# Performance work log

Measured on AMD Instinct MI355X. Metric: run time of the kernel, lower is better.

The kernel has to match this reference:

```python
import jax, jax.numpy as jnp
import numpy as np

K = 16          # patch_size
P2 = 256        # patch_size**2
D_PD = 512      # learned base dictionary atoms (D_out_lam_pd)
D_LAM = 112     # adaptive atoms from sdict, = 8*14 (D_out_lam)
DD = D_PD + D_LAM  # 624
T = 5
INDICE = 112
MIN_V, MAX_V = 0.0, 1.0


def _idx(H, W, k, stride):
    oh = (H - k) // stride + 1
    ow = (W - k) // stride + 1
    r = jnp.arange(k)[:, None] + stride * jnp.arange(oh)[None, :]  # [k, oh]
    c = jnp.arange(k)[:, None] + stride * jnp.arange(ow)[None, :]  # [k, ow]
    return r[:, None, :, None], c[None, :, None, :], oh, ow


def _unfold(x, k, stride):
    # torch.nn.Unfold: [N, C*k*k, L] with (C, kh, kw) channel order, row-major L
    N, C, H, W = x.shape
    r, c, oh, ow = _idx(H, W, k, stride)
    return x[:, :, r, c].reshape(N, C * k * k, oh * ow)


def _fold(p, H, W, k):
    # torch.nn.functional.fold (col2im) with stride 1, overlap-add
    N, ckk, L = p.shape
    r, c, oh, ow = _idx(H, W, k, 1)
    C = ckk // (k * k)
    out = jnp.zeros((N, C, H, W), p.dtype)
    return out.at[:, :, r, c].add(p.reshape(N, C, k, k, oh, ow))


def _mlp(x, ws):
    # Linear + clamp(min=0) chain, no relu after last layer (dropout = eval identity)
    for w, b in ws[:-1]:
        x = jnp.maximum(x @ w + b, 0.0)
    w, b = ws[-1]
    return x @ w + b


def _cbam(x, w1, w2, conv_w):
    # standard CBAM: channel attention (shared MLP on avg+max pool) then 7x7 spatial attention
    def mlp(v):
        return jnp.maximum(v @ w1, 0.0) @ w2
    ca = jax.nn.sigmoid(mlp(x.mean(axis=(2, 3))) + mlp(x.max(axis=(2, 3))))
    x = x * ca[:, :, None, None]
    s = jnp.stack([x.mean(axis=1), x.max(axis=1)], axis=1)  # [N,2,h,w]
    sa = jax.lax.conv_general_dilated(s, conv_w, (1, 1), [(3, 3), (3, 3)],
                                      dimension_numbers=('NCHW', 'OIHW', 'NCHW'))
    return x * jax.nn.sigmoid(sa)


def _soft(x, l):
    return jnp.sign(x) * jnp.maximum(jnp.abs(x) - l, 0.0)


def _stage(img, Dict, c, sd_ws, ca1, ca2, saw, lam_ws, pd_ws, w_ws):
    N, C, H, W = img.shape
    uf = _unfold(img, K, 1).transpose(0, 2, 1)     # [N, L, 256]
    uf1 = _unfold(img, K, 8).transpose(0, 2, 1)    # [N, L1, 256]
    step = uf1.shape[1] // INDICE                  # static under jit
    ext = uf1[:, ::step, :][:, :INDICE, :]         # [N, 112, 256]
    sd = _mlp(ext, sd_ws)                          # linears1..4
    sd = sd / jnp.maximum(jnp.linalg.norm(sd, axis=-1, keepdims=True), 1e-12)
    sd = _cbam(sd.transpose(0, 2, 1).reshape(N, P2, 8, 14), ca1, ca2, saw)
    sd = sd.reshape(N, P2, INDICE)                 # [N, 256, 112]
    Dcat = jnp.concatenate([jnp.broadcast_to(Dict, (N,) + Dict.shape), sd], axis=-1)  # [N,256,624]
    # thresholds: l = cat(lpd, ls)
    thr = jnp.concatenate([_mlp(uf, pd_ws) / c, _mlp(uf, lam_ws) / c], axis=-1)  # [N,L,624]
    y = uf @ Dcat                                  # [N, L, 624]
    # S = (I - D^T D / c)^T; D^T D is symmetric so the transpose is a no-op
    S = jnp.eye(DD, dtype=img.dtype) - (Dcat.transpose(0, 2, 1) @ Dcat) / c
    z = _soft(y, thr)
    for _ in range(T):  # LISTA unrolled iterations (T static)
        z = _soft(z @ S + y / c, thr)
    Wg = jax.nn.sigmoid(_mlp(uf, w_ws))            # [N, L, 256]
    x_pred = jnp.clip(z @ Dcat.transpose(0, 2, 1), MIN_V, MAX_V) * Wg
    num = _fold(x_pred.transpose(0, 2, 1), H, W, K)
    den = _fold(Wg.transpose(0, 2, 1), H, W, K)    # fold of W * ones
    return num / den


def _forward(x, Dict, c, s1w, s1b, s2w, s2b, s3w, s3b, s4w, s4b, caw1, caw2, saw,
             a1w, a1b, a2w, a2b, a3w, a3b, p1w, p1b, p2w, p2b, p3w, p3b,
             b1w, b1b, b2w, b2b, b3w, b3b, q1w, q1b, q2w, q2b, q3w, q3b,
             w1w, w1b, w2w, w2b, w3w, w3b):
    sd_ws = [(s1w, s1b), (s2w, s2b), (s3w, s3b), (s4w, s4b)]
    w_ws = [(w1w, w1b), (w2w, w2b), (w3w, w3b)]
    res = _stage(x, Dict, c, sd_ws, caw1, caw2, saw,
                 [(a1w, a1b), (a2w, a2b), (a3w, a3b)],
                 [(p1w, p1b), (p2w, p2b), (p3w, p3b)], w_ws)
    res = _stage(res, Dict, c, sd_ws, caw1, caw2, saw,
                 [(b1w, b1b), (b2w, b2b), (b3w, b3b)],
                 [(q1w, q1b), (q2w, q2b), (q3w, q3b)], w_ws)
    return res


def setup_inputs() -> dict:
    key = jax.random.key(0)
    ks = iter(jax.random.split(key, 40))
    d = {}
    d['x'] = jax.random.uniform(next(ks), (2, 1, 128, 128), jnp.float32)
    Dm = jax.random.normal(next(ks), (P2, D_PD), jnp.float32)
    d['Dict'] = Dm / jnp.linalg.norm(Dm, axis=0, keepdims=True)  # unit-norm atoms
    d['c'] = jnp.asarray(10.0, jnp.float32)  # c > ||D^T D||_2
    dims = {'s1': (256, 512), 's2': (512, 1024), 's3': (1024, 512), 's4': (512, 256),
            'a1': (256, 1024), 'a2': (1024, 512), 'a3': (512, 112),
            'p1': (256, 1024), 'p2': (1024, 512), 'p3': (512, 512),
            'b1': (256, 1024), 'b2': (1024, 512), 'b3': (512, 112),
            'q1': (256, 1024), 'q2': (1024, 512), 'q3': (512, 512),
            'w1': (256, 1024), 'w2': (1024, 512), 'w3': (512, 256)}
    for name, (i, o) in dims.items():
        d[name + 'w'] = jax.random.normal(next(ks), (i, o), jnp.float32) / np.float32(np.sqrt(i))
        d[name + 'b'] = jnp.zeros((o,), jnp.float32)
    d['caw1'] = jax.random.normal(next(ks), (256, 512), jnp.float32) / np.float32(16.0)
    d['caw2'] = jax.random.normal(next(ks), (512, 256), jnp.float32) / np.float32(np.sqrt(512))
    d['saw'] = jax.random.normal(next(ks), (1, 2, 7, 7), jnp.float32) * np.float32(0.1)
    return d


def reference(x, Dict, c, s1w, s1b, s2w, s2b, s3w, s3b, s4w, s4b, caw1, caw2, saw,
              a1w, a1b, a2w, a2b, a3w, a3b, p1w, p1b, p2w, p2b, p3w, p3b,
              b1w, b1b, b2w, b2b, b3w, b3b, q1w, q1b, q2w, q2b, q3w, q3b,
              w1w, w1b, w2w, w2b, w3w, w3b):
    return _forward(x, Dict, c, s1w, s1b, s2w, s2b, s3w, s3b, s4w, s4b, caw1, caw2, saw,
                    a1w, a1b, a2w, a2b, a3w, a3b, p1w, p1b, p2w, p2b, p3w, p3b,
                    b1w, b1b, b2w, b2b, b3w, b3b, q1w, q1b, q2w, q2b, q3w, q3b,
                    w1w, w1b, w2w, w2b, w3w, w3b)
```

## Files before the change

### kernel.cpp

```cpp
#include <hip/hip_runtime.h>
#include <hip/hip_bf16.h>
#include <math.h>

#define L_LOC 12769
#define NB 2
#define NLR (NB * L_LOC)

typedef short short8v __attribute__((ext_vector_type(8)));
typedef float f32x4 __attribute__((ext_vector_type(4)));
typedef __hip_bfloat16 bf16;

__device__ __forceinline__ float softf(float x, float l) {
  float a = fmaxf(fabsf(x) - l, 0.0f);
  return x > 0.0f ? a : (x < 0.0f ? -a : 0.0f);
}
__device__ __forceinline__ float sigf(float x) { return 1.0f / (1.0f + expf(-x)); }
__device__ __forceinline__ void split2(float v, bf16& h, bf16& l) {
  h = __float2bfloat16(v);
  l = __float2bfloat16(v - __bfloat162float(h));
}

__global__ __launch_bounds__(256) void sdmlp_k(
    const float* __restrict__ img,
    const float* __restrict__ w1, const float* __restrict__ b1,
    const float* __restrict__ w2, const float* __restrict__ b2,
    const float* __restrict__ w3, const float* __restrict__ b3,
    const float* __restrict__ w4, const float* __restrict__ b4,
    float* __restrict__ sd)
{
  __shared__ float A_[4][1024];
  __shared__ float B_[4][1024];
  __shared__ float red[4][4];
  const int r0 = blockIdx.x * 4;
  const int t = threadIdx.x;
#pragma unroll
  for (int rr = 0; rr < 4; ++rr) {
    int r = r0 + rr;
    int n = r / 112, e = r - n * 112;
    int l1 = 2 * e, i1 = l1 / 15, j1 = l1 - i1 * 15;
    A_[rr][t] = img[n * 16384 + (8 * i1 + (t >> 4)) * 128 + 8 * j1 + (t & 15)];
  }
  __syncthreads();
  {
    float acc[4][2];
#pragma unroll
    for (int rr = 0; rr < 4; ++rr) { acc[rr][0] = b1[t]; acc[rr][1] = b1[t + 256]; }
#pragma unroll 4
    for (int k = 0; k < 256; ++k) {
      float w0 = w1[k * 512 + t], w1v = w1[k * 512 + t + 256];
#pragma unroll
      for (int rr = 0; rr < 4; ++rr) {
        float a = A_[rr][k];
        acc[rr][0] = fmaf(a, w0, acc[rr][0]);
        acc[rr][1] = fmaf(a, w1v, acc[rr][1]);
      }
    }
#pragma unroll
    for (int rr = 0; rr < 4; ++rr) {
      B_[rr][t] = fmaxf(acc[rr][0], 0.0f);
      B_[rr][t + 256] = fmaxf(acc[rr][1], 0.0f);
    }
  }
  __syncthreads();
  {
    float acc[4][4];
#pragma unroll
    for (int rr = 0; rr < 4; ++rr)
#pragma unroll
      for (int j = 0; j < 4; ++j) acc[rr][j] = b2[t + j * 256];
#pragma unroll 4
    for (int k = 0; k < 512; ++k) {
      float w0 = w2[k * 1024 + t], w1v = w2[k * 1024 + t + 256];
      float w2v = w2[k * 1024 + t + 512], w3v = w2[k * 1024 + t + 768];
#pragma unroll
      for (int rr = 0; rr < 4; ++rr) {
        float a = B_[rr][k];
        acc[rr][0] = fmaf(a, w0, acc[rr][0]);
        acc[rr][1] = fmaf(a, w1v, acc[rr][1]);
        acc[rr][2] = fmaf(a, w2v, acc[rr][2]);
        acc[rr][3] = fmaf(a, w3v, acc[rr][3]);
      }
    }
    __syncthreads();
#pragma unroll
    for (int rr = 0; rr < 4; ++rr)
#pragma unroll
      for (int j = 0; j < 4; ++j) A_[rr][t + j * 256] = fmaxf(acc[rr][j], 0.0f);
  }
  __syncthreads();
  {
    float acc[4][2];
#pragma unroll
    for (int rr = 0; rr < 4; ++rr) { acc[rr][0] = b3[t]; acc[rr][1] = b3[t + 256]; }
#pragma unroll 4
    for (int k = 0; k < 1024; ++k) {
      float w0 = w3[k * 512 + t], w1v = w3[k * 512 + t + 256];
#pragma unroll
      for (int rr = 0; rr < 4; ++rr) {
        float a = A_[rr][k];
        acc[rr][0] = fmaf(a, w0, acc[rr][0]);
        acc[rr][1] = fmaf(a, w1v, acc[rr][1]);
      }
    }
    __syncthreads();
#pragma unroll
    for (int rr = 0; rr < 4; ++rr) {
      B_[rr][t] = fmaxf(acc[rr][0], 0.0f);
      B_[rr][t + 256] = fmaxf(acc[rr][1], 0.0f);
    }
  }
  __syncthreads();
  float v[4];
#pragma unroll
  for (int rr = 0; rr < 4; ++rr) v[rr] = b4[t];
#pragma unroll 4
  for (int k = 0; k < 512; ++k) {
    float w = w4[k * 256 + t];
#pragma unroll
    for (int rr = 0; rr < 4; ++rr) v[rr] = fmaf(B_[rr][k], w, v[rr]);
  }
  float ss[4];
#pragma unroll
  for (int rr = 0; rr < 4; ++rr) ss[rr] = v[rr] * v[rr];
#pragma unroll
  for (int o = 1; o < 64; o <<= 1)
#pragma unroll
    for (int rr = 0; rr < 4; ++rr) ss[rr] += __shfl_xor(ss[rr], o);
  if ((t & 63) == 0)
#pragma unroll
    for (int rr = 0; rr < 4; ++rr) red[t >> 6][rr] = ss[rr];
  __syncthreads();
#pragma unroll
  for (int rr = 0; rr < 4; ++rr) {
    float s = red[0][rr] + red[1][rr] + red[2][rr] + red[3][rr];
    float sc = 1.0f / fmaxf(sqrtf(s), 1e-12f);
    sd[(r0 + rr) * 256 + t] = v[rr] * sc;
  }
}

enum { ME_RELU = 0, ME_SCALE = 1, ME_SIG = 2, ME_Y = 3, ME_SOFT = 4, ME_XP = 5, ME_SMAT = 6 };

template <int EPI, int TERMS, int WLO>
__global__ __launch_bounds__(256) void mgemm_k(
    const bf16* __restrict__ A, int lda, size_t aOff,
    const bf16* __restrict__ B0, const bf16* __restrict__ B1, int ldb, size_t bOff,
    void* __restrict__ Cv, int ldc, size_t cOff,
    bf16* __restrict__ Zp,
    const float* __restrict__ bias,
    const float* __restrict__ E1, const float* __restrict__ E2, int lde,
    const float* __restrict__ cptr, int bRow, int Rc, int r0, int N, int K)
{
  const int NPA = (TERMS >= 3) ? 2 : 1;
  const int NPB = (TERMS >= 2) ? 2 : 1;
  __shared__ char As[(TERMS >= 3) ? 2 : 1][8192];
  __shared__ char Bs[(TERMS >= 2) ? 2 : 1][8192];
  const int t = threadIdx.x;
  const int lane = t & 63, wv = t >> 6;
  const int wr = wv >> 1, wc = wv & 1;
  const int m0 = blockIdx.x * 128, n0 = blockIdx.y * 128;
  const int nb = (m0 >= bRow) ? 1 : 0;
  const bf16* __restrict__ Bt = nb ? B1 : B0;
  const int row16 = lane & 15, kg = lane >> 4;
  const int grow = t >> 2;
  const int gcol = (t & 3) * 8;
  f32x4 acc[4][4];
#pragma unroll
  for (int i = 0; i < 4; ++i)
#pragma unroll
    for (int j = 0; j < 4; ++j) { acc[i][j][0] = 0.f; acc[i][j][1] = 0.f; acc[i][j][2] = 0.f; acc[i][j][3] = 0.f; }

  for (int k0 = 0; k0 < K; k0 += 32) {
#pragma unroll
    for (int h = 0; h < NPA; ++h)
#pragma unroll
      for (int i = 0; i < 2; ++i) {
        const bf16* ga = A + h * aOff + (size_t)(m0 + i * 64 + grow) * lda + k0 + gcol;
        __builtin_amdgcn_global_load_lds(
            (const __attribute__((address_space(1))) void*)ga,
            (__attribute__((address_space(3))) void*)(As[h] + i * 4096 + wv * 1024), 16, 0, 0);
      }
#pragma unroll
    for (int h = 0; h < NPB; ++h)
#pragma unroll
      for (int i = 0; i < 2; ++i) {
        const bf16* gb = Bt + h * bOff + (size_t)(n0 + i * 64 + grow) * ldb + k0 + gcol;
        __builtin_amdgcn_global_load_lds(
            (const __attribute__((address_space(1))) void*)gb,
            (__attribute__((address_space(3))) void*)(Bs[h] + i * 4096 + wv * 1024), 16, 0, 0);
      }
    __syncthreads();
    short8v ah[4], al[4], bh[4], bl[4];
#pragma unroll
    for (int mi = 0; mi < 4; ++mi) {
      int o = (wr * 64 + mi * 16 + row16) * 64 + kg * 16;
      ah[mi] = *(const short8v*)(As[0] + o);
      if (TERMS >= 3) al[mi] = *(const short8v*)(As[NPA - 1] + o);
    }
#pragma unroll
    for (int ni = 0; ni < 4; ++ni) {
      int o = (wc * 64 + ni * 16 + row16) * 64 + kg * 16;
      bh[ni] = *(const short8v*)(Bs[0] + o);
      if (TERMS >= 2) bl[ni] = *(const short8v*)(Bs[NPB - 1] + o);
    }
#pragma unroll
    for (int mi = 0; mi < 4; ++mi)
#pragma unroll
      for (int ni = 0; ni < 4; ++ni) {
        if (TERMS >= 2)
          acc[mi][ni] = __builtin_amdgcn_mfma_f32_16x16x32_bf16(ah[mi], bl[ni], acc[mi][ni], 0, 0, 0);
        if (TERMS >= 3)
          acc[mi][ni] = __builtin_amdgcn_mfma_f32_16x16x32_bf16(al[mi], bh[ni], acc[mi][ni], 0, 0, 0);
        acc[mi][ni] = __builtin_amdgcn_mfma_f32_16x16x32_bf16(ah[mi], bh[ni], acc[mi][ni], 0, 0, 0);
      }
    __syncthreads();
  }

  float invc = 1.0f;
  if (EPI == ME_SCALE || EPI == ME_SOFT || EPI == ME_SMAT) invc = 1.0f / cptr[0];
  bf16* Cb = (bf16*)Cv;
  float* Cf = (float*)Cv;
#pragma unroll
  for (int ni = 0; ni < 4; ++ni) {
    int col = n0 + wc * 64 + ni * 16 + row16;
    const bool colok = col < N;
    float bv = 0.0f;
    if ((EPI == ME_RELU || EPI == ME_SCALE || EPI == ME_SIG) && colok) bv = bias[col];
#pragma unroll
    for (int mi = 0; mi < 4; ++mi) {
      int rowb = m0 + wr * 64 + mi * 16 + kg * 4;
#pragma unroll
      for (int r = 0; r < 4; ++r) {
        int row = rowb + r;
        float v = acc[mi][ni][r];
        if (EPI == ME_RELU) {
          if (colok) {
            float o = fmaxf(v + bv, 0.0f);
            size_t ci = (size_t)row * ldc + col;
            if (WLO) {
              bf16 h, l; split2(o, h, l);
              Cb[ci] = h; Cb[ci + cOff] = l;
            } else {
              Cb[ci] = __float2bfloat16(o);
            }
          }
        } else if (EPI == ME_SCALE) {
          if (colok) Cf[(size_t)row * ldc + col] = (v + bv) * invc;
        } else if (EPI == ME_SIG) {
          if (colok) {
            int rl = row - nb * bRow;
            if (rl < Rc && rl >= 0)
              Cf[(size_t)col * NLR + (size_t)nb * L_LOC + r0 + rl] = sigf(v + bv);
          }
        } else if (EPI == ME_Y) {
          if (colok) {
            size_t e = (size_t)row * lde + col;
            Cf[(size_t)row * ldc + col] = v;
            Zp[(size_t)row * 640 + col] = __float2bfloat16(softf(v, E1[e]));
          }
        } else if (EPI == ME_SOFT) {
          if (colok) {
            size_t e = (size_t)row * lde + col;
            Cb[(size_t)row * ldc + col] = __float2bfloat16(softf(v + E1[e] * invc, E2[e]));
          }
        } else if (EPI == ME_XP) {
          int rl = row - nb * bRow;
          if (colok && rl < Rc && rl >= 0) {
            size_t g = (size_t)col * NLR + (size_t)nb * L_LOC + r0 + rl;
            Cf[g] = fminf(fmaxf(v, 0.0f), 1.0f) * E1[g];
          }
        } else {
          if (row < Rc && colok)
            Cf[(size_t)row * ldc + col] = (row == col ? 1.0f : 0.0f) - v * invc;
        }
      }
    }
  }
}

static void mgemm(hipStream_t st, int EPI, int wlo,
                  const bf16* A, int lda, size_t aOff,
                  const bf16* B0, const bf16* B1, int ldb, size_t bOff,
                  void* C, int ldc, size_t cOff,
                  bf16* Zp,
                  const float* bias, const float* E1, const float* E2, int lde,
                  const float* cptr, int bRow, int Rc, int r0,
                  int Mp, int N, int K)
{
  dim3 grid(Mp / 128, (N + 127) / 128), blk(256);
#define MG(ep, tm, wl) mgemm_k<ep, tm, wl><<<grid, blk, 0, st>>>(A, lda, aOff, B0, B1, ldb, bOff, C, ldc, cOff, Zp, bias, E1, E2, lde, cptr, bRow, Rc, r0, N, K)
  switch (EPI) {
    case ME_RELU:  if (wlo) MG(ME_RELU, 1, 1); else MG(ME_RELU, 1, 0); break;
    case ME_SCALE: MG(ME_SCALE, 3, 0); break;
    case ME_SIG:   MG(ME_SIG, 1, 0); break;
    case ME_Y:     MG(ME_Y, 3, 0); break;
    case ME_SOFT:  MG(ME_SOFT, 2, 0); break;
    case ME_XP:    MG(ME_XP, 2, 0); break;
    case ME_SMAT:  MG(ME_SMAT, 3, 0); break;
  }
#undef MG
}

struct WTable {
  const float* src[15];
  bf16* dst[15];
  int K[15], N[15], Kp[15], Np[15];
  int base[16];
};

__global__ void wtransall_k(WTable w) {
  int idx = blockIdx.x * 256 + threadIdx.x;
  if (idx >= w.base[15]) return;
  int s = 0;
  while (s < 14 && idx >= w.base[s + 1]) ++s;
  int li = idx - w.base[s];
  int Kp = w.Kp[s];
  int n = li / Kp, k = li - n * Kp;
  float v = (n < w.N[s] && k < w.K[s]) ? w.src[s][(size_t)k * w.N[s] + n] : 0.0f;
  bf16 h, l; split2(v, h, l);
  w.dst[s][li] = h;
  w.dst[s][li + (size_t)w.Np[s] * Kp] = l;
}

__global__ void dcatconv_k(const float* __restrict__ Dict, const float* __restrict__ Dc,
                           bf16* __restrict__ Db, bf16* __restrict__ DbT) {
  int idx = blockIdx.x * 256 + threadIdx.x;
  if (idx >= 327680) return;
  int n = idx / 163840, r = idx - n * 163840;
  int p = r / 640, a = r - p * 640;
  float v = 0.0f;
  if (a < 512)      v = Dict[p * 512 + a];
  else if (a < 624) v = Dc[(size_t)n * 159744 + p * 624 + a];
  bf16 h, l; split2(v, h, l);
  size_t base = (size_t)n * 327680;
  Db[base + p * 640 + a] = h;
  Db[base + 163840 + p * 640 + a] = l;
  DbT[base + (size_t)a * 256 + p] = h;
  DbT[base + 163840 + (size_t)a * 256 + p] = l;
}

__global__ void sconv_k(const float* __restrict__ Sf, bf16* __restrict__ Sb) {
  int idx = blockIdx.x * 256 + threadIdx.x;
  if (idx >= 819200) return;
  int n = idx / 409600, r = idx - n * 409600;
  int i = r / 640, j = r - i * 640;
  float v = (i < 624 && j < 624) ? Sf[(size_t)n * 389376 + i * 624 + j] : 0.0f;
  bf16 h, l; split2(v, h, l);
  size_t base = (size_t)n * 819200;
  Sb[base + r] = h; Sb[base + 409600 + r] = l;
}

__global__ void unfold_k(const float* __restrict__ img, bf16* __restrict__ uf,
                         int r0, int Rc, int bRowc, size_t pOff) {
  int bi = blockIdx.x;
  int nb = bi >= Rc;
  int rl = nb ? bi - Rc : bi;
  int row = nb * bRowc + rl;
  int p = threadIdx.x;
  int l = r0 + rl;
  int i0 = l / 113, j0 = l - i0 * 113;
  float v = img[nb * 16384 + (i0 + (p >> 4)) * 128 + j0 + (p & 15)];
  bf16 h, lo; split2(v, h, lo);
  size_t o = (size_t)row * 256 + p;
  uf[o] = h; uf[o + pOff] = lo;
}

__global__ __launch_bounds__(1024) void cbam_k(
    const float* __restrict__ sd, const float* __restrict__ w1,
    const float* __restrict__ w2, const float* __restrict__ saw,
    float* __restrict__ Dcat)
{
  __shared__ float mv[512], xv[512], hm[1024], hx[1024], ca[512];
  __shared__ float smean[224], smax[224];
  const int t = threadIdx.x;
  if (t < 512) {
    int n = t >> 8, ch = t & 255;
    float s = 0.0f, m = -INFINITY;
    for (int e = 0; e < 112; ++e) {
      float v = sd[(n * 112 + e) * 256 + ch];
      s += v; m = fmaxf(m, v);
    }
    mv[t] = s * (1.0f / 112.0f);
    xv[t] = m;
  }
  __syncthreads();
  {
    int n = t >> 9, o = t & 511;
    float sm = 0.0f, sx = 0.0f;
    for (int i = 0; i < 256; ++i) {
      float w = w1[i * 512 + o];
      sm += mv[n * 256 + i] * w;
      sx += xv[n * 256 + i] * w;
    }
    hm[t] = fmaxf(sm, 0.0f);
    hx[t] = fmaxf(sx, 0.0f);
  }
  __syncthreads();
  if (t < 512) {
    int n = t >> 8, ch = t & 255;
    float s = 0.0f;
    for (int o = 0; o < 512; ++o) s += (hm[n * 512 + o] + hx[n * 512 + o]) * w2[o * 256 + ch];
    ca[t] = sigf(s);
  }
  __syncthreads();
  if (t < 224) {
    int n = t / 112, s = t % 112;
    float sum = 0.0f, mx = -INFINITY;
    for (int ch = 0; ch < 256; ++ch) {
      float v = sd[(n * 112 + s) * 256 + ch] * ca[n * 256 + ch];
      Dcat[(size_t)n * 159744 + ch * 624 + 512 + s] = v;
      sum += v; mx = fmaxf(mx, v);
    }
    smean[t] = sum * (1.0f / 256.0f);
    smax[t] = mx;
  }
  __syncthreads();
  if (t < 224) {
    int n = t / 112, s = t % 112;
    int h = s / 14, w = s % 14;
    float acc = 0.0f;
    for (int dh = 0; dh < 7; ++dh) {
      int hh = h + dh - 3; if (hh < 0 || hh >= 8) continue;
      for (int dw = 0; dw < 7; ++dw) {
        int ww = w + dw - 3; if (ww < 0 || ww >= 14) continue;
        int sp = hh * 14 + ww;
        acc += smean[n * 112 + sp] * saw[dh * 7 + dw] + smax[n * 112 + sp] * saw[49 + dh * 7 + dw];
      }
    }
    float sg = sigf(acc);
    for (int ch = 0; ch < 256; ++ch) Dcat[(size_t)n * 159744 + ch * 624 + 512 + s] *= sg;
  }
}

__global__ void folddiv_k(const float* __restrict__ xpT, const float* __restrict__ wgT,
                          float* __restrict__ out) {
  int idx = blockIdx.x * 256 + threadIdx.x;
  if (idx >= 32768) return;
  int n = idx >> 14, rem = idx & 16383;
  int i = rem >> 7, j = rem & 127;
  float num = 0.0f, den = 0.0f;
  int kh0 = (i - 112 > 0) ? i - 112 : 0;
  int kh1 = (i < 15) ? i : 15;
  int kw0 = (j - 112 > 0) ? j - 112 : 0;
  int kw1 = (j < 15) ? j : 15;
  for (int kh = kh0; kh <= kh1; ++kh)
    for (int kw = kw0; kw <= kw1; ++kw) {
      int l = (i - kh) * 113 + (j - kw);
      size_t base = (size_t)(kh * 16 + kw) * NLR + (size_t)n * L_LOC + l;
      num += xpT[base];
      den += wgT[base];
    }
  out[idx] = num / den;
}

struct Bufs {
  float *xp, *wg, *Dcat_f, *S_f, *sd, *res;
  bf16 *Db, *DbT, *Sb;
  bf16 *uf, *h1, *h2, *z, *zn;
  float *thr, *y;
  size_t ufO, h1O, h2O;
  int R;
};

static void run_stage(hipStream_t st, const float* const* in, const float* img,
                      float* outimg, int pd0, int lam0,
                      bf16* const* WtPd, bf16* const* WtLam, bf16* const* WtW,
                      const Bufs& b)
{
  const float* cptr = in[2];
  sdmlp_k<<<dim3(56), dim3(256), 0, st>>>(img, in[3], in[4], in[5], in[6],
                                          in[7], in[8], in[9], in[10], b.sd);
  cbam_k<<<dim3(1), dim3(1024), 0, st>>>(b.sd, in[41], in[42], in[43], b.Dcat_f);
  dcatconv_k<<<dim3(1280), dim3(256), 0, st>>>(in[1], b.Dcat_f, b.Db, b.DbT);
  for (int n = 0; n < NB; ++n) {
    const bf16* Dt = b.DbT + (size_t)n * 327680;
    mgemm(st, ME_SMAT, 0, Dt, 256, 163840, Dt, Dt, 256, 163840,
          b.S_f + (size_t)n * 389376, 624, 0, 0,
          0, 0, 0, 0, cptr, 1 << 30, 624, 0, 640, 624, 256);
  }
  sconv_k<<<dim3(3200), dim3(256), 0, st>>>(b.S_f, b.Sb);

  for (int r0 = 0; r0 < L_LOC; r0 += b.R) {
    int Rc = L_LOC - r0; if (Rc > b.R) Rc = b.R;
    int bRowc = ((Rc + 127) / 128) * 128;
    int Mp = 2 * bRowc;
    unfold_k<<<dim3(2 * Rc), dim3(256), 0, st>>>(img, b.uf, r0, Rc, bRowc, b.ufO);
    mgemm(st, ME_RELU, 0, b.uf, 256, b.ufO, WtPd[0], WtPd[0], 256, 1024 * 256, b.h1, 1024, b.h1O,
          0, in[pd0 + 1], 0, 0, 0, cptr, bRowc, Rc, r0, Mp, 1024, 256);
    mgemm(st, ME_RELU, 1, b.h1, 1024, b.h1O, WtPd[1], WtPd[1], 1024, 512 * 1024, b.h2, 512, b.h2O,
          0, in[pd0 + 3], 0, 0, 0, cptr, bRowc, Rc, r0, Mp, 512, 1024);
    mgemm(st, ME_SCALE, 0, b.h2, 512, b.h2O, WtPd[2], WtPd[2], 512, 512 * 512, b.thr, 640, 0,
          0, in[pd0 + 5], 0, 0, 0, cptr, bRowc, Rc, r0, Mp, 512, 512);
    mgemm(st, ME_RELU, 0, b.uf, 256, b.ufO, WtLam[0], WtLam[0], 256, 1024 * 256, b.h1, 1024, b.h1O,
          0, in[lam0 + 1], 0, 0, 0, cptr, bRowc, Rc, r0, Mp, 1024, 256);
    mgemm(st, ME_RELU, 1, b.h1, 1024, b.h1O, WtLam[1], WtLam[1], 1024, 512 * 1024, b.h2, 512, b.h2O,
          0, in[lam0 + 3], 0, 0, 0, cptr, bRowc, Rc, r0, Mp, 512, 1024);
    mgemm(st, ME_SCALE, 0, b.h2, 512, b.h2O, WtLam[2], WtLam[2], 512, 128 * 512, b.thr + 512, 640, 0,
          0, in[lam0 + 5], 0, 0, 0, cptr, bRowc, Rc, r0, Mp, 112, 512);
    mgemm(st, ME_RELU, 0, b.uf, 256, b.ufO, WtW[0], WtW[0], 256, 1024 * 256, b.h1, 1024, b.h1O,
          0, in[36], 0, 0, 0, cptr, bRowc, Rc, r0, Mp, 1024, 256);
    mgemm(st, ME_RELU, 1, b.h1, 1024, b.h1O, WtW[1], WtW[1], 1024, 512 * 1024, b.h2, 512, b.h2O,
          0, in[38], 0, 0, 0, cptr, bRowc, Rc, r0, Mp, 512, 1024);
    mgemm(st, ME_SIG, 0, b.h2, 512, b.h2O, WtW[2], WtW[2], 512, 256 * 512, b.wg, 0, 0,
          0, in[40], 0, 0, 0, cptr, bRowc, Rc, r0, Mp, 256, 512);
    mgemm(st, ME_Y, 0, b.uf, 256, b.ufO, b.DbT, b.DbT + 327680, 256, 163840, b.y, 640, 0,
          b.z, 0, b.thr, 0, 640, cptr, bRowc, Rc, r0, Mp, 624, 256);
    bf16* zi = b.z; bf16* zo = b.zn;
    for (int it = 0; it < 5; ++it) {
      mgemm(st, ME_SOFT, 0, zi, 640, 0, b.Sb, b.Sb + 819200, 640, 409600, zo, 640, 0,
            0, 0, b.y, b.thr, 640, cptr, bRowc, Rc, r0, Mp, 624, 640);
      bf16* tmp = zi; zi = zo; zo = tmp;
    }
    mgemm(st, ME_XP, 0, zi, 640, 0, b.Db, b.Db + 327680, 640, 163840, b.xp, 0, 0,
          0, 0, b.wg, 0, 0, cptr, bRowc, Rc, r0, Mp, 256, 640);
  }
  folddiv_k<<<dim3(128), dim3(256), 0, st>>>(b.xp, b.wg, outimg);
}

extern "C" void kernel_launch(void* const* d_in, const int* in_sizes, int n_in,
                              void* d_out, int out_size, void* d_ws, size_t ws_size,
                              hipStream_t stream)
{
  (void)in_sizes; (void)n_in; (void)out_size;
  const float* const* in = (const float* const*)d_in;
  char* base = (char*)d_ws;
  size_t off = 0;
  auto allocf = [&](size_t nelem) -> float* {
    float* p = (float*)(base + off);
    off += ((nelem * 4 + 255) / 256) * 256;
    return p;
  };
  auto allocb2 = [&](size_t nelem) -> bf16* {
    bf16* p = (bf16*)(base + off);
    off += ((nelem * 2 * 2 + 255) / 256) * 256;
    return p;
  };
  auto allocb1 = [&](size_t nelem) -> bf16* {
    bf16* p = (bf16*)(base + off);
    off += ((nelem * 2 + 255) / 256) * 256;
    return p;
  };
  Bufs b;
  b.xp = allocf((size_t)NLR * 256);
  b.wg = allocf((size_t)NLR * 256);
  b.Dcat_f = allocf(2 * 256 * 624);
  b.S_f = allocf(2 * 624 * 624);
  b.sd = allocf(224 * 256);
  b.res = allocf(2 * 16384);
  b.Db = allocb2(2 * 163840);
  b.DbT = allocb2(2 * 163840);
  b.Sb = allocb2(2 * 409600);

  bf16 *Wa[3], *Wp[3], *Wb[3], *Wq[3], *Ww[3];
  struct WDesc { bf16** slot; int inIdx; int K, N, Kp, Np; };
  WDesc wd[15] = {
    {&Wa[0], 11, 256, 1024, 256, 1024}, {&Wa[1], 13, 1024, 512, 1024, 512}, {&Wa[2], 15, 512, 112, 512, 128},
    {&Wp[0], 17, 256, 1024, 256, 1024}, {&Wp[1], 19, 1024, 512, 1024, 512}, {&Wp[2], 21, 512, 512, 512, 512},
    {&Wb[0], 23, 256, 1024, 256, 1024}, {&Wb[1], 25, 1024, 512, 1024, 512}, {&Wb[2], 27, 512, 112, 512, 128},
    {&Wq[0], 29, 256, 1024, 256, 1024}, {&Wq[1], 31, 1024, 512, 1024, 512}, {&Wq[2], 33, 512, 512, 512, 512},
    {&Ww[0], 35, 256, 1024, 256, 1024}, {&Ww[1], 37, 1024, 512, 1024, 512}, {&Ww[2], 39, 512, 256, 512, 256},
  };
  WTable wt;
  int tot = 0;
  for (int i = 0; i < 15; ++i) {
    *wd[i].slot = allocb2((size_t)wd[i].Np * wd[i].Kp);
    wt.src[i] = in[wd[i].inIdx];
    wt.dst[i] = *wd[i].slot;
    wt.K[i] = wd[i].K; wt.N[i] = wd[i].N; wt.Kp[i] = wd[i].Kp; wt.Np[i] = wd[i].Np;
    wt.base[i] = tot;
    tot += wd[i].Np * wd[i].Kp;
  }
  wt.base[15] = tot;
  wtransall_k<<<dim3((tot + 255) / 256), dim3(256), 0, stream>>>(wt);

  long long avail = (long long)ws_size - (long long)off - (1 << 20);
  long long perrow2 = 2LL * (12800 + 64);
  int R = 12800;
  if (avail / perrow2 < 12800) R = (int)(avail / perrow2);
  R &= ~127;
  if (R < 128) R = 128;
  b.R = R;
  size_t rows2 = (size_t)2 * R;
  b.uf = allocb2(rows2 * 256);  b.ufO = rows2 * 256;
  b.h1 = allocb1(rows2 * 1024); b.h1O = 0;
  b.h2 = allocb2(rows2 * 512);  b.h2O = rows2 * 512;
  b.z = allocb1(rows2 * 640);
  b.zn = allocb1(rows2 * 640);
  b.thr = allocf(rows2 * 640);
  b.y = allocf(rows2 * 640);

  run_stage(stream, in, in[0], b.res, 17, 11, Wp, Wa, Ww, b);
  run_stage(stream, in, b.res, (float*)d_out, 29, 23, Wq, Wb, Ww, b);
}
```

Baseline: 3.260 ms.

## Fuse first-layer MLP GEMMs, move sdict MLP to MFMA, fold S conversion into epilogue

```diff
diff --git a/kernel.cpp b/kernel.cpp
--- a/kernel.cpp
+++ b/kernel.cpp
@@ -5,6 +5,7 @@
 #define L_LOC 12769
 #define NB 2
 #define NLR (NB * L_LOC)
+#define NW 20
 
 typedef short short8v __attribute__((ext_vector_type(8)));
 typedef float f32x4 __attribute__((ext_vector_type(4)));
@@ -20,125 +21,8 @@
   l = __float2bfloat16(v - __bfloat162float(h));
 }
 
-__global__ __launch_bounds__(256) void sdmlp_k(
-    const float* __restrict__ img,
-    const float* __restrict__ w1, const float* __restrict__ b1,
-    const float* __restrict__ w2, const float* __restrict__ b2,
-    const float* __restrict__ w3, const float* __restrict__ b3,
-    const float* __restrict__ w4, const float* __restrict__ b4,
-    float* __restrict__ sd)
-{
-  __shared__ float A_[4][1024];
-  __shared__ float B_[4][1024];
-  __shared__ float red[4][4];
-  const int r0 = blockIdx.x * 4;
-  const int t = threadIdx.x;
-#pragma unroll
-  for (int rr = 0; rr < 4; ++rr) {
-    int r = r0 + rr;
-    int n = r / 112, e = r - n * 112;
-    int l1 = 2 * e, i1 = l1 / 15, j1 = l1 - i1 * 15;
-    A_[rr][t] = img[n * 16384 + (8 * i1 + (t >> 4)) * 128 + 8 * j1 + (t & 15)];
-  }
-  __syncthreads();
-  {
-    float acc[4][2];
-#pragma unroll
-    for (int rr = 0; rr < 4; ++rr) { acc[rr][0] = b1[t]; acc[rr][1] = b1[t + 256]; }
-#pragma unroll 4
-    for (int k = 0; k < 256; ++k) {
-      float w0 = w1[k * 512 + t], w1v = w1[k * 512 + t + 256];
-#pragma unroll
-      for (int rr = 0; rr < 4; ++rr) {
-        float a = A_[rr][k];
-        acc[rr][0] = fmaf(a, w0, acc[rr][0]);
-        acc[rr][1] = fmaf(a, w1v, acc[rr][1]);
-      }
-    }
-#pragma unroll
-    for (int rr = 0; rr < 4; ++rr) {
-      B_[rr][t] = fmaxf(acc[rr][0], 0.0f);
-      B_[rr][t + 256] = fmaxf(acc[rr][1], 0.0f);
-    }
-  }
-  __syncthreads();
-  {
-    float acc[4][4];
-#pragma unroll
-    for (int rr = 0; rr < 4; ++rr)
-#pragma unroll
-      for (int j = 0; j < 4; ++j) acc[rr][j] = b2[t + j * 256];
-#pragma unroll 4
-    for (int k = 0; k < 512; ++k) {
-      float w0 = w2[k * 1024 + t], w1v = w2[k * 1024 + t + 256];
-      float w2v = w2[k * 1024 + t + 512], w3v = w2[k * 1024 + t + 768];
-#pragma unroll
-      for (int rr = 0; rr < 4; ++rr) {
-        float a = B_[rr][k];
-        acc[rr][0] = fmaf(a, w0, acc[rr][0]);
-        acc[rr][1] = fmaf(a, w1v, acc[rr][1]);
-        acc[rr][2] = fmaf(a, w2v, acc[rr][2]);
-        acc[rr][3] = fmaf(a, w3v, acc[rr][3]);
-      }
-    }
-    __syncthreads();
-#pragma unroll
-    for (int rr = 0; rr < 4; ++rr)
-#pragma unroll
-      for (int j = 0; j < 4; ++j) A_[rr][t + j * 256] = fmaxf(acc[rr][j], 0.0f);
-  }
-  __syncthreads();
-  {
-    float acc[4][2];
-#pragma unroll
-    for (int rr = 0; rr < 4; ++rr) { acc[rr][0] = b3[t]; acc[rr][1] = b3[t + 256]; }
-#pragma unroll 4
-    for (int k = 0; k < 1024; ++k) {
-      float w0 = w3[k * 512 + t], w1v = w3[k * 512 + t + 256];
-#pragma unroll
-      for (int rr = 0; rr < 4; ++rr) {
-        float a = A_[rr][k];
-        acc[rr][0] = fmaf(a, w0, acc[rr][0]);
-        acc[rr][1] = fmaf(a, w1v, acc[rr][1]);
-      }
-    }
-    __syncthreads();
-#pragma unroll
-    for (int rr = 0; rr < 4; ++rr) {
-      B_[rr][t] = fmaxf(acc[rr][0], 0.0f);
-      B_[rr][t + 256] = fmaxf(acc[rr][1], 0.0f);
-    }
-  }
-  __syncthreads();
-  float v[4];
-#pragma unroll
-  for (int rr = 0; rr < 4; ++rr) v[rr] = b4[t];
-#pragma unroll 4
-  for (int k = 0; k < 512; ++k) {
-    float w = w4[k * 256 + t];
-#pragma unroll
-    for (int rr = 0; rr < 4; ++rr) v[rr] = fmaf(B_[rr][k], w, v[rr]);
-  }
-  float ss[4];
-#pragma unroll
-  for (int rr = 0; rr < 4; ++rr) ss[rr] = v[rr] * v[rr];
-#pragma unroll
-  for (int o = 1; o < 64; o <<= 1)
-#pragma unroll
-    for (int rr = 0; rr < 4; ++rr) ss[rr] += __shfl_xor(ss[rr], o);
-  if ((t & 63) == 0)
-#pragma unroll
-    for (int rr = 0; rr < 4; ++rr) red[t >> 6][rr] = ss[rr];
-  __syncthreads();
-#pragma unroll
-  for (int rr = 0; rr < 4; ++rr) {
-    float s = red[0][rr] + red[1][rr] + red[2][rr] + red[3][rr];
-    float sc = 1.0f / fmaxf(sqrtf(s), 1e-12f);
-    sd[(r0 + rr) * 256 + t] = v[rr] * sc;
-  }
-}
-
-enum { ME_RELU = 0, ME_SCALE = 1, ME_SIG = 2, ME_Y = 3, ME_SOFT = 4, ME_XP = 5, ME_SMAT = 6 };
+enum { ME_RELU = 0, ME_SCALE = 1, ME_SIG = 2, ME_Y = 3, ME_SOFT = 4, ME_XP = 5,
+       ME_SMAT = 6, ME_LIN = 7 };
 
 template <int EPI, int TERMS, int WLO>
 __global__ __launch_bounds__(256) void mgemm_k(
@@ -224,7 +108,8 @@
     int col = n0 + wc * 64 + ni * 16 + row16;
     const bool colok = col < N;
     float bv = 0.0f;
-    if ((EPI == ME_RELU || EPI == ME_SCALE || EPI == ME_SIG) && colok) bv = bias[col];
+    if ((EPI == ME_RELU || EPI == ME_SCALE || EPI == ME_SIG || EPI == ME_LIN) && colok)
+      bv = bias[col];
 #pragma unroll
     for (int mi = 0; mi < 4; ++mi) {
       int rowb = m0 + wr * 64 + mi * 16 + kg * 4;
@@ -243,6 +128,8 @@
               Cb[ci] = __float2bfloat16(o);
             }
           }
+        } else if (EPI == ME_LIN) {
+          if (colok && row < Rc) Cf[(size_t)row * ldc + col] = v + bv;
         } else if (EPI == ME_SCALE) {
           if (colok) Cf[(size_t)row * ldc + col] = (v + bv) * invc;
         } else if (EPI == ME_SIG) {
@@ -269,15 +156,17 @@
             Cf[g] = fminf(fmaxf(v, 0.0f), 1.0f) * E1[g];
           }
         } else {
-          if (row < Rc && colok)
-            Cf[(size_t)row * ldc + col] = (row == col ? 1.0f : 0.0f) - v * invc;
+          float o = (row < 624 && col < 624) ? ((row == col ? 1.0f : 0.0f) - v * invc) : 0.0f;
+          bf16 h, l; split2(o, h, l);
+          size_t ci = (size_t)row * ldc + col;
+          Cb[ci] = h; Cb[ci + cOff] = l;
         }
       }
     }
   }
 }
 
-static void mgemm(hipStream_t st, int EPI, int wlo,
+static void mgemm(hipStream_t st, int EPI, int terms, int wlo,
                   const bf16* A, int lda, size_t aOff,
                   const bf16* B0, const bf16* B1, int ldb, size_t bOff,
                   void* C, int ldc, size_t cOff,
@@ -288,37 +177,74 @@
 {
   dim3 grid(Mp / 128, (N + 127) / 128), blk(256);
 #define MG(ep, tm, wl) mgemm_k<ep, tm, wl><<<grid, blk, 0, st>>>(A, lda, aOff, B0, B1, ldb, bOff, C, ldc, cOff, Zp, bias, E1, E2, lde, cptr, bRow, Rc, r0, N, K)
-  switch (EPI) {
-    case ME_RELU:  if (wlo) MG(ME_RELU, 1, 1); else MG(ME_RELU, 1, 0); break;
-    case ME_SCALE: MG(ME_SCALE, 3, 0); break;
-    case ME_SIG:   MG(ME_SIG, 1, 0); break;
-    case ME_Y:     MG(ME_Y, 3, 0); break;
-    case ME_SOFT:  MG(ME_SOFT, 2, 0); break;
-    case ME_XP:    MG(ME_XP, 2, 0); break;
-    case ME_SMAT:  MG(ME_SMAT, 3, 0); break;
-  }
+  if (EPI == ME_RELU && terms == 1 && !wlo) { MG(ME_RELU, 1, 0); }
+  else if (EPI == ME_RELU && terms == 1)    { MG(ME_RELU, 1, 1); }
+  else if (EPI == ME_RELU)                  { MG(ME_RELU, 3, 1); }
+  else if (EPI == ME_LIN)                   { MG(ME_LIN, 3, 0); }
+  else if (EPI == ME_SCALE)                 { MG(ME_SCALE, 3, 0); }
+  else if (EPI == ME_SIG)                   { MG(ME_SIG, 1, 0); }
+  else if (EPI == ME_Y)                     { MG(ME_Y, 3, 0); }
+  else if (EPI == ME_SOFT)                  { MG(ME_SOFT, 2, 0); }
+  else if (EPI == ME_XP)                    { MG(ME_XP, 2, 0); }
+  else                                      { MG(ME_SMAT, 3, 0); }
 #undef MG
 }
 
 struct WTable {
-  const float* src[15];
-  bf16* dst[15];
-  int K[15], N[15], Kp[15], Np[15];
-  int base[16];
+  const float* src[NW];
+  bf16* dst[NW];
+  int K[NW], N[NW], Kp[NW], Np[NW];
+  long long loOff[NW];
+  int base[NW + 1];
 };
 
 __global__ void wtransall_k(WTable w) {
   int idx = blockIdx.x * 256 + threadIdx.x;
-  if (idx >= w.base[15]) return;
+  if (idx >= w.base[NW]) return;
   int s = 0;
-  while (s < 14 && idx >= w.base[s + 1]) ++s;
+  while (s < NW - 1 && idx >= w.base[s + 1]) ++s;
   int li = idx - w.base[s];
   int Kp = w.Kp[s];
   int n = li / Kp, k = li - n * Kp;
   float v = (n < w.N[s] && k < w.K[s]) ? w.src[s][(size_t)k * w.N[s] + n] : 0.0f;
   bf16 h, l; split2(v, h, l);
   w.dst[s][li] = h;
-  w.dst[s][li + (size_t)w.Np[s] * Kp] = l;
+  w.dst[s][li + w.loOff[s]] = l;
+}
+
+__global__ void biascat_k(const float* p1, const float* a1, const float* w1b,
+                          const float* q1, const float* b1,
+                          float* c1, float* c2) {
+  int i = blockIdx.x * 256 + threadIdx.x;
+  if (i >= 3072) return;
+  int br = i >> 10, o = i & 1023;
+  c1[i] = br == 0 ? p1[o] : (br == 1 ? a1[o] : w1b[o]);
+  c2[i] = br == 0 ? q1[o] : (br == 1 ? b1[o] : w1b[o]);
+}
+
+__global__ void extb_k(const float* __restrict__ img, bf16* __restrict__ dst) {
+  int idx = blockIdx.x * 256 + threadIdx.x;
+  int row = idx >> 8, p = idx & 255;
+  float v = 0.0f;
+  if (row < 224) {
+    int n = row / 112, e = row - n * 112;
+    int l1 = 2 * e, i1 = l1 / 15, j1 = l1 - i1 * 15;
+    v = img[n * 16384 + (8 * i1 + (p >> 4)) * 128 + 8 * j1 + (p & 15)];
+  }
+  bf16 h, l; split2(v, h, l);
+  dst[idx] = h; dst[idx + 65536] = l;
+}
+
+__global__ void rownorm224_k(float* sd) {
+  int r = blockIdx.x, t = threadIdx.x;
+  float v[4], s = 0.0f;
+#pragma unroll
+  for (int j = 0; j < 4; ++j) { v[j] = sd[r * 256 + t + 64 * j]; s += v[j] * v[j]; }
+#pragma unroll
+  for (int o = 1; o < 64; o <<= 1) s += __shfl_xor(s, o);
+  float sc = 1.0f / fmaxf(sqrtf(s), 1e-12f);
+#pragma unroll
+  for (int j = 0; j < 4; ++j) sd[r * 256 + t + 64 * j] = v[j] * sc;
 }
 
 __global__ void dcatconv_k(const float* __restrict__ Dict, const float* __restrict__ Dc,
@@ -336,17 +262,6 @@
   Db[base + 163840 + p * 640 + a] = l;
   DbT[base + (size_t)a * 256 + p] = h;
   DbT[base + 163840 + (size_t)a * 256 + p] = l;
-}
-
-__global__ void sconv_k(const float* __restrict__ Sf, bf16* __restrict__ Sb) {
-  int idx = blockIdx.x * 256 + threadIdx.x;
-  if (idx >= 819200) return;
-  int n = idx / 409600, r = idx - n * 409600;
-  int i = r / 640, j = r - i * 640;
-  float v = (i < 624 && j < 624) ? Sf[(size_t)n * 389376 + i * 624 + j] : 0.0f;
-  bf16 h, l; split2(v, h, l);
-  size_t base = (size_t)n * 819200;
-  Sb[base + r] = h; Sb[base + 409600 + r] = l;
 }
 
 __global__ void unfold_k(const float* __restrict__ img, bf16* __restrict__ uf,
@@ -453,65 +368,71 @@
 }
 
 struct Bufs {
-  float *xp, *wg, *Dcat_f, *S_f, *sd, *res;
+  float *xp, *wg, *Dcat_f, *sd, *res;
   bf16 *Db, *DbT, *Sb;
+  bf16 *extb, *sdh1, *sdh2, *sdh3;
   bf16 *uf, *h1, *h2, *z, *zn;
   float *thr, *y;
-  size_t ufO, h1O, h2O;
+  size_t ufO, h2O;
   int R;
 };
 
 static void run_stage(hipStream_t st, const float* const* in, const float* img,
                       float* outimg, int pd0, int lam0,
+                      const bf16* Wcat, const float* bcat,
                       bf16* const* WtPd, bf16* const* WtLam, bf16* const* WtW,
-                      const Bufs& b)
+                      bf16* const* Ws, const Bufs& b)
 {
   const float* cptr = in[2];
-  sdmlp_k<<<dim3(56), dim3(256), 0, st>>>(img, in[3], in[4], in[5], in[6],
-                                          in[7], in[8], in[9], in[10], b.sd);
+  const int BIG = 1 << 30;
+  extb_k<<<dim3(256), dim3(256), 0, st>>>(img, b.extb);
+  mgemm(st, ME_RELU, 3, 1, b.extb, 256, 65536, Ws[0], Ws[0], 256, 512 * 256,
+        b.sdh1, 512, 256 * 512, 0, in[4], 0, 0, 0, cptr, BIG, 224, 0, 256, 512, 256);
+  mgemm(st, ME_RELU, 3, 1, b.sdh1, 512, 256 * 512, Ws[1], Ws[1], 512, 1024 * 512,
+        b.sdh2, 1024, 256 * 1024, 0, in[6], 0, 0, 0, cptr, BIG, 224, 0, 256, 1024, 512);
+  mgemm(st, ME_RELU, 3, 1, b.sdh2, 1024, 256 * 1024, Ws[2], Ws[2], 1024, 512 * 1024,
+        b.sdh3, 512, 256 * 512, 0, in[8], 0, 0, 0, cptr, BIG, 224, 0, 256, 512, 1024);
+  mgemm(st, ME_LIN, 3, 0, b.sdh3, 512, 256 * 512, Ws[3], Ws[3], 512, 256 * 512,
+        b.sd, 256, 0, 0, in[10], 0, 0, 0, cptr, BIG, 224, 0, 256, 256, 512);
+  rownorm224_k<<<dim3(224), dim3(64), 0, st>>>(b.sd);
   cbam_k<<<dim3(1), dim3(1024), 0, st>>>(b.sd, in[41], in[42], in[43], b.Dcat_f);
   dcatconv_k<<<dim3(1280), dim3(256), 0, st>>>(in[1], b.Dcat_f, b.Db, b.DbT);
   for (int n = 0; n < NB; ++n) {
     const bf16* Dt = b.DbT + (size_t)n * 327680;
-    mgemm(st, ME_SMAT, 0, Dt, 256, 163840, Dt, Dt, 256, 163840,
-          b.S_f + (size_t)n * 389376, 624, 0, 0,
-          0, 0, 0, 0, cptr, 1 << 30, 624, 0, 640, 624, 256);
-  }
-  sconv_k<<<dim3(3200), dim3(256), 0, st>>>(b.S_f, b.Sb);
+    mgemm(st, ME_SMAT, 3, 0, Dt, 256, 163840, Dt, Dt, 256, 163840,
+          b.Sb + (size_t)n * 819200, 640, 409600, 0,
+          0, 0, 0, 0, cptr, BIG, 624, 0, 640, 640, 256);
+  }
 
   for (int r0 = 0; r0 < L_LOC; r0 += b.R) {
     int Rc = L_LOC - r0; if (Rc > b.R) Rc = b.R;
     int bRowc = ((Rc + 127) / 128) * 128;
     int Mp = 2 * bRowc;
     unfold_k<<<dim3(2 * Rc), dim3(256), 0, st>>>(img, b.uf, r0, Rc, bRowc, b.ufO);
-    mgemm(st, ME_RELU, 0, b.uf, 256, b.ufO, WtPd[0], WtPd[0], 256, 1024 * 256, b.h1, 1024, b.h1O,
-          0, in[pd0 + 1], 0, 0, 0, cptr, bRowc, Rc, r0, Mp, 1024, 256);
-    mgemm(st, ME_RELU, 1, b.h1, 1024, b.h1O, WtPd[1], WtPd[1], 1024, 512 * 1024, b.h2, 512, b.h2O,
-          0, in[pd0 + 3], 0, 0, 0, cptr, bRowc, Rc, r0, Mp, 512, 1024);
-    mgemm(st, ME_SCALE, 0, b.h2, 512, b.h2O, WtPd[2], WtPd[2], 512, 512 * 512, b.thr, 640, 0,
-          0, in[pd0 + 5], 0, 0, 0, cptr, bRowc, Rc, r0, Mp, 512, 512);
-    mgemm(st, ME_RELU, 0, b.uf, 256, b.ufO, WtLam[0], WtLam[0], 256, 1024 * 256, b.h1, 1024, b.h1O,
-          0, in[lam0 + 1], 0, 0, 0, cptr, bRowc, Rc, r0, Mp, 1024, 256);
-    mgemm(st, ME_RELU, 1, b.h1, 1024, b.h1O, WtLam[1], WtLam[1], 1024, 512 * 1024, b.h2, 512, b.h2O,
-          0, in[lam0 + 3], 0, 0, 0, cptr, bRowc, Rc, r0, Mp, 512, 1024);
-    mgemm(st, ME_SCALE, 0, b.h2, 512, b.h2O, WtLam[2], WtLam[2], 512, 128 * 512, b.thr + 512, 640, 0,
-          0, in[lam0 + 5], 0, 0, 0, cptr, bRowc, Rc, r0, Mp, 112, 512);
-    mgemm(st, ME_RELU, 0, b.uf, 256, b.ufO, WtW[0], WtW[0], 256, 1024 * 256, b.h1, 1024, b.h1O,
-          0, in[36], 0, 0, 0, cptr, bRowc, Rc, r0, Mp, 1024, 256);
-    mgemm(st, ME_RELU, 1, b.h1, 1024, b.h1O, WtW[1], WtW[1], 1024, 512 * 1024, b.h2, 512, b.h2O,
-          0, in[38], 0, 0, 0, cptr, bRowc, Rc, r0, Mp, 512, 1024);
-    mgemm(st, ME_SIG, 0, b.h2, 512, b.h2O, WtW[2], WtW[2], 512, 256 * 512, b.wg, 0, 0,
-          0, in[40], 0, 0, 0, cptr, bRowc, Rc, r0, Mp, 256, 512);
-    mgemm(st, ME_Y, 0, b.uf, 256, b.ufO, b.DbT, b.DbT + 327680, 256, 163840, b.y, 640, 0,
-          b.z, 0, b.thr, 0, 640, cptr, bRowc, Rc, r0, Mp, 624, 256);
+    mgemm(st, ME_RELU, 1, 0, b.uf, 256, b.ufO, Wcat, Wcat, 256, 3072 * 256,
+          b.h1, 3072, 0, 0, bcat, 0, 0, 0, cptr, bRowc, Rc, r0, Mp, 3072, 256);
+    mgemm(st, ME_RELU, 1, 1, b.h1, 3072, 0, WtPd[1], WtPd[1], 1024, 512 * 1024,
+          b.h2, 512, b.h2O, 0, in[pd0 + 3], 0, 0, 0, cptr, bRowc, Rc, r0, Mp, 512, 1024);
+    mgemm(st, ME_SCALE, 3, 0, b.h2, 512, b.h2O, WtPd[2], WtPd[2], 512, 512 * 512,
+          b.thr, 640, 0, 0, in[pd0 + 5], 0, 0, 0, cptr, bRowc, Rc, r0, Mp, 512, 512);
+    mgemm(st, ME_RELU, 1, 1, b.h1 + 1024, 3072, 0, WtLam[1], WtLam[1], 1024, 512 * 1024,
+          b.h2, 512, b.h2O, 0, in[lam0 + 3], 0, 0, 0, cptr, bRowc, Rc, r0, Mp, 512, 1024);
+    mgemm(st, ME_SCALE, 3, 0, b.h2, 512, b.h2O, WtLam[2], WtLam[2], 512, 128 * 512,
+          b.thr + 512, 640, 0, 0, in[lam0 + 5], 0, 0, 0, cptr, bRowc, Rc, r0, Mp, 112, 512);
+    mgemm(st, ME_RELU, 1, 1, b.h1 + 2048, 3072, 0, WtW[1], WtW[1], 1024, 512 * 1024,
+          b.h2, 512, b.h2O, 0, in[38], 0, 0, 0, cptr, bRowc, Rc, r0, Mp, 512, 1024);
+    mgemm(st, ME_SIG, 1, 0, b.h2, 512, b.h2O, WtW[2], WtW[2], 512, 256 * 512,
+          b.wg, 0, 0, 0, in[40], 0, 0, 0, cptr, bRowc, Rc, r0, Mp, 256, 512);
+    mgemm(st, ME_Y, 3, 0, b.uf, 256, b.ufO, b.DbT, b.DbT + 327680, 256, 163840,
+          b.y, 640, 0, b.z, 0, b.thr, 0, 640, cptr, bRowc, Rc, r0, Mp, 624, 256);
     bf16* zi = b.z; bf16* zo = b.zn;
     for (int it = 0; it < 5; ++it) {
-      mgemm(st, ME_SOFT, 0, zi, 640, 0, b.Sb, b.Sb + 819200, 640, 409600, zo, 640, 0,
-            0, 0, b.y, b.thr, 640, cptr, bRowc, Rc, r0, Mp, 624, 640);
+      mgemm(st, ME_SOFT, 2, 0, zi, 640, 0, b.Sb, b.Sb + 819200, 640, 409600,
+            zo, 640, 0, 0, 0, b.y, b.thr, 640, cptr, bRowc, Rc, r0, Mp, 624, 640);
       bf16* tmp = zi; zi = zo; zo = tmp;
     }
-    mgemm(st, ME_XP, 0, zi, 640, 0, b.Db, b.Db + 327680, 640, 163840, b.xp, 0, 0,
-          0, 0, b.wg, 0, 0, cptr, bRowc, Rc, r0, Mp, 256, 640);
+    mgemm(st, ME_XP, 2, 0, zi, 640, 0, b.Db, b.Db + 327680, 640, 163840,
+          b.xp, 0, 0, 0, 0, b.wg, 0, 0, cptr, bRowc, Rc, r0, Mp, 256, 640);
   }
   folddiv_k<<<dim3(128), dim3(256), 0, st>>>(b.xp, b.wg, outimg);
 }
@@ -543,37 +464,61 @@
   b.xp = allocf((size_t)NLR * 256);
   b.wg = allocf((size_t)NLR * 256);
   b.Dcat_f = allocf(2 * 256 * 624);
-  b.S_f = allocf(2 * 624 * 624);
   b.sd = allocf(224 * 256);
   b.res = allocf(2 * 16384);
   b.Db = allocb2(2 * 163840);
   b.DbT = allocb2(2 * 163840);
   b.Sb = allocb2(2 * 409600);
-
-  bf16 *Wa[3], *Wp[3], *Wb[3], *Wq[3], *Ww[3];
-  struct WDesc { bf16** slot; int inIdx; int K, N, Kp, Np; };
-  WDesc wd[15] = {
-    {&Wa[0], 11, 256, 1024, 256, 1024}, {&Wa[1], 13, 1024, 512, 1024, 512}, {&Wa[2], 15, 512, 112, 512, 128},
-    {&Wp[0], 17, 256, 1024, 256, 1024}, {&Wp[1], 19, 1024, 512, 1024, 512}, {&Wp[2], 21, 512, 512, 512, 512},
-    {&Wb[0], 23, 256, 1024, 256, 1024}, {&Wb[1], 25, 1024, 512, 1024, 512}, {&Wb[2], 27, 512, 112, 512, 128},
-    {&Wq[0], 29, 256, 1024, 256, 1024}, {&Wq[1], 31, 1024, 512, 1024, 512}, {&Wq[2], 33, 512, 512, 512, 512},
-    {&Ww[0], 35, 256, 1024, 256, 1024}, {&Ww[1], 37, 1024, 512, 1024, 512}, {&Ww[2], 39, 512, 256, 512, 256},
+  b.extb = allocb2(256 * 256);
+  b.sdh1 = allocb2(256 * 512);
+  b.sdh2 = allocb2(256 * 1024);
+  b.sdh3 = allocb2(256 * 512);
+  bf16* Wcat1 = allocb1(2 * 3072 * 256);
+  bf16* Wcat2 = allocb1(2 * 3072 * 256);
+  float* bcat1 = allocf(3072);
+  float* bcat2 = allocf(3072);
+
+  bf16 *Wa[3], *Wp[3], *Wb[3], *Wq[3], *Ww[3], *Ws[4];
+  WTable wt;
+  int ne = 0, tot = 0;
+  auto addw = [&](const float* src, bf16* dst, int K, int N, int Kp, int Np, long long loOff) {
+    wt.src[ne] = src; wt.dst[ne] = dst;
+    wt.K[ne] = K; wt.N[ne] = N; wt.Kp[ne] = Kp; wt.Np[ne] = Np;
+    wt.loOff[ne] = loOff; wt.base[ne] = tot;
+    tot += Np * Kp; ++ne;
   };
-  WTable wt;
-  int tot = 0;
-  for (int i = 0; i < 15; ++i) {
+  int sdK[4] = {256, 512, 1024, 512}, sdN[4] = {512, 1024, 512, 256}, sdIdx[4] = {3, 5, 7, 9};
+  for (int i = 0; i < 4; ++i) {
+    Ws[i] = allocb2((size_t)sdN[i] * sdK[i]);
+    addw(in[sdIdx[i]], Ws[i], sdK[i], sdN[i], sdK[i], sdN[i], (long long)sdN[i] * sdK[i]);
+  }
+  struct WD { bf16** slot; int idx, K, N, Kp, Np; };
+  WD wd[10] = {
+    {&Wa[1], 13, 1024, 512, 1024, 512}, {&Wa[2], 15, 512, 112, 512, 128},
+    {&Wp[1], 19, 1024, 512, 1024, 512}, {&Wp[2], 21, 512, 512, 512, 512},
+    {&Wb[1], 25, 1024, 512, 1024, 512}, {&Wb[2], 27, 512, 112, 512, 128},
+    {&Wq[1], 31, 1024, 512, 1024, 512}, {&Wq[2], 33, 512, 512, 512, 512},
+    {&Ww[1], 37, 1024, 512, 1024, 512}, {&Ww[2], 39, 512, 256, 512, 256},
+  };
+  for (int i = 0; i < 10; ++i) {
     *wd[i].slot = allocb2((size_t)wd[i].Np * wd[i].Kp);
-    wt.src[i] = in[wd[i].inIdx];
-    wt.dst[i] = *wd[i].slot;
-    wt.K[i] = wd[i].K; wt.N[i] = wd[i].N; wt.Kp[i] = wd[i].Kp; wt.Np[i] = wd[i].Np;
-    wt.base[i] = tot;
-    tot += wd[i].Np * wd[i].Kp;
-  }
-  wt.base[15] = tot;
+    addw(in[wd[i].idx], *wd[i].slot, wd[i].K, wd[i].N, wd[i].Kp, wd[i].Np,
+         (long long)wd[i].Np * wd[i].Kp);
+  }
+  const long long catLo = 3072LL * 256;
+  addw(in[17], Wcat1 + 0 * 262144, 256, 1024, 256, 1024, catLo);
+  addw(in[11], Wcat1 + 1 * 262144, 256, 1024, 256, 1024, catLo);
+  addw(in[35], Wcat1 + 2 * 262144, 256, 1024, 256, 1024, catLo);
+  addw(in[29], Wcat2 + 0 * 262144, 256, 1024, 256, 1024, catLo);
+  addw(in[23], Wcat2 + 1 * 262144, 256, 1024, 256, 1024, catLo);
+  addw(in[35], Wcat2 + 2 * 262144, 256, 1024, 256, 1024, catLo);
+  wt.base[NW] = tot;
   wtransall_k<<<dim3((tot + 255) / 256), dim3(256), 0, stream>>>(wt);
+  biascat_k<<<dim3(12), dim3(256), 0, stream>>>(in[18], in[12], in[36], in[30], in[24],
+                                                bcat1, bcat2);
 
   long long avail = (long long)ws_size - (long long)off - (1 << 20);
-  long long perrow2 = 2LL * (12800 + 64);
+  long long perrow2 = 2LL * (16896 + 64);
   int R = 12800;
   if (avail / perrow2 < 12800) R = (int)(avail / perrow2);
   R &= ~127;
@@ -581,13 +526,13 @@
   b.R = R;
   size_t rows2 = (size_t)2 * R;
   b.uf = allocb2(rows2 * 256);  b.ufO = rows2 * 256;
-  b.h1 = allocb1(rows2 * 1024); b.h1O = 0;
+  b.h1 = allocb1(rows2 * 3072);
   b.h2 = allocb2(rows2 * 512);  b.h2O = rows2 * 512;
   b.z = allocb1(rows2 * 640);
   b.zn = allocb1(rows2 * 640);
   b.thr = allocf(rows2 * 640);
   b.y = allocf(rows2 * 640);
 
-  run_stage(stream, in, in[0], b.res, 17, 11, Wp, Wa, Ww, b);
-  run_stage(stream, in, b.res, (float*)d_out, 29, 23, Wq, Wb, Ww, b);
-}
+  run_stage(stream, in, in[0], b.res, 17, 11, Wcat1, bcat1, Wp, Wa, Ww, Ws, b);
+  run_stage(stream, in, b.res, (float*)d_out, 29, 23, Wcat2, bcat2, Wq, Wb, Ww, Ws, b);
+}
```

After: 3.845 ms. +17.9%, slower.
